# Performance work log

Measured on AMD Instinct MI355X. Metric: run time of the kernel, lower is better.

## Reference

```python
import jax, jax.numpy as jnp
import numpy as np

EPS = 1e-12  # torch F.normalize eps


def setup_inputs() -> dict:
    key = jax.random.key(0)
    k1, k2 = jax.random.split(key)
    b, c, n, h, w = 4, 64, 25, 64, 64
    dims = 64
    x = jax.random.normal(k1, (b, c, n, h, w), dtype=jnp.float32)
    # 1x1 conv weight: Conv2d(channels, dims*3, 1, bias=False) -> [3*dims, channels]
    W = jax.random.normal(k2, (3 * dims, c), dtype=jnp.float32) * 0.05
    return {"x": x, "W": W}


def reference(x, W):
    b, c, n, h, w = x.shape
    N = n * h * w
    # 1x1 conv over channel dim (applied per (b, n) slice == plain channel matmul)
    qkv = jnp.einsum('oc,bcnhw->bonhw', W, x)  # [b, 3d, n, h, w]
    q, k, v = jnp.split(qkv, 3, axis=1)        # each [b, d, n, h, w]
    d = q.shape[1]
    q = q.reshape(b, d, N)  # b c (n h w)
    k = k.reshape(b, d, N)
    v = v.reshape(b, d, N)
    # L2-normalize each channel across the token axis (torch normalize semantics)
    qn = q / jnp.maximum(jnp.linalg.norm(q, axis=-1, keepdims=True), EPS)
    kn = k / jnp.maximum(jnp.linalg.norm(k, axis=-1, keepdims=True), EPS)
    # channel-wise cross-covariance attention: [b, d, d]
    att = jnp.einsum('bdN,beN->bde', qn, kn)
    att = jax.nn.softmax(att, axis=-1)
    out = jnp.einsum('bde,beN->bdN', att, v)   # [b, d, N]
    return out.reshape(b, d, n, h, w)
```

## Files before the change

kernel.cpp:

```cpp
#include <hip/hip_runtime.h>
#include <hip/hip_bf16.h>


#define BATCH 4
#define CH 64
#define NTOK 102400
#define DIM 64

#define NBLK_G 200
#define TOK_PER_G 512
#define GBLK_OUT 320
#define TILES_PER_BLK 5

static const size_t OFF_PART = 0;
static const size_t OFF_G    = (size_t)BATCH * NBLK_G * 4096;
static const size_t OFF_T1   = OFF_G  + (size_t)BATCH * 4096;
static const size_t OFF_INV  = OFF_T1 + (size_t)BATCH * 4096;
static const size_t OFF_MT   = OFF_INV + (size_t)BATCH * 128;
static const size_t WS_FLOATS_FULL = OFF_MT + (size_t)BATCH * 4096;

static const size_t SOFF_G   = 0;
static const size_t SOFF_T1  = (size_t)BATCH * 4096;
static const size_t SOFF_INV = SOFF_T1 + (size_t)BATCH * 4096;
static const size_t SOFF_MT  = SOFF_INV + (size_t)BATCH * 128;

typedef __attribute__((ext_vector_type(8))) short short8v;
typedef __attribute__((ext_vector_type(4))) float f32x4;

__global__ void k_zero(float* __restrict__ p, int n) {
  int i = blockIdx.x * blockDim.x + threadIdx.x;
  if (i < n) p[i] = 0.f;
}

__device__ __forceinline__ short f2bf(float f) {
  unsigned u = __builtin_bit_cast(unsigned, f);
  unsigned r = (u + 0x7fffu + ((u >> 16) & 1u)) >> 16;
  return (short)r;
}
__device__ __forceinline__ float bf2f(short s) {
  unsigned u = ((unsigned)(unsigned short)s) << 16;
  return __builtin_bit_cast(float, u);
}

template <bool ATOMIC>
__global__ __launch_bounds__(256, 3) void k_gram(const float* __restrict__ x,
                                                 float* __restrict__ dstG) {
  __shared__ short his[2][4096];
  __shared__ short los[2][4096];
  __shared__ float p2t[64][65];
  const int b = blockIdx.y, blk = blockIdx.x;
  const int tid = threadIdx.x;
  const int w = tid >> 6, lane = tid & 63;
  const int col = lane & 15, kh = lane >> 4;
  const int cs = tid >> 2, tq = tid & 3;

  const float* xb = x + (size_t)b * CH * NTOK;
  const int t0 = blk * TOK_PER_G;

  f32x4 a1[4], a2[4];
#pragma unroll
  for (int cb = 0; cb < 4; ++cb)
#pragma unroll
    for (int r = 0; r < 4; ++r) { a1[cb][r] = 0.f; a2[cb][r] = 0.f; }

  const int sbase = cs * 64;
  const int s0 = ((2 * tq) ^ (cs & 7)) << 3;
  const int s1 = ((2 * tq + 1) ^ (cs & 7)) << 3;

  {
    const float* src = xb + (size_t)cs * NTOK + t0 + 16 * tq;
    float4 v0 = *(const float4*)(src);
    float4 v1 = *(const float4*)(src + 4);
    float4 v2 = *(const float4*)(src + 8);
    float4 v3 = *(const float4*)(src + 12);
    float f[16] = {v0.x, v0.y, v0.z, v0.w, v1.x, v1.y, v1.z, v1.w,
                   v2.x, v2.y, v2.z, v2.w, v3.x, v3.y, v3.z, v3.w};
    short8v h01, h23, l01, l23;
#pragma unroll
    for (int j = 0; j < 8; ++j) {
      short h = f2bf(f[j]);     h01[j] = h; l01[j] = f2bf(f[j] - bf2f(h));
      short g = f2bf(f[j + 8]); h23[j] = g; l23[j] = f2bf(f[j + 8] - bf2f(g));
    }
    *(short8v*)&his[0][sbase + s0] = h01;
    *(short8v*)&his[0][sbase + s1] = h23;
    *(short8v*)&los[0][sbase + s0] = l01;
    *(short8v*)&los[0][sbase + s1] = l23;
  }
  __syncthreads();

#pragma unroll 1
  for (int i = 0; i < TOK_PER_G / 64; ++i) {
    const int cur = i & 1;
    const bool more = (i + 1) < TOK_PER_G / 64;
    float4 n0, n1, n2, n3;
    if (more) {
      const float* src = xb + (size_t)cs * NTOK + t0 + (i + 1) * 64 + 16 * tq;
      n0 = *(const float4*)(src);
      n1 = *(const float4*)(src + 4);
      n2 = *(const float4*)(src + 8);
      n3 = *(const float4*)(src + 12);
    }
    const short* hp = his[cur];
    const short* lp = los[cur];
#pragma unroll
    for (int kc = 0; kc < 2; ++kc) {
      const int g = kc * 4 + kh;
      const int rA = 16 * w + col;
      const short8v A = *(const short8v*)&hp[rA * 64 + ((g ^ (rA & 7)) << 3)];
#pragma unroll
      for (int cb = 0; cb < 4; ++cb) {
        const int rB = 16 * cb + col;
        const int off = rB * 64 + ((g ^ (rB & 7)) << 3);
        const short8v Bh = *(const short8v*)&hp[off];
        const short8v Bl = *(const short8v*)&lp[off];
        a1[cb] = __builtin_amdgcn_mfma_f32_16x16x32_bf16(A, Bh, a1[cb], 0, 0, 0);
        a2[cb] = __builtin_amdgcn_mfma_f32_16x16x32_bf16(A, Bl, a2[cb], 0, 0, 0);
      }
    }
    if (more) {
      const int nxt = cur ^ 1;
      float f[16] = {n0.x, n0.y, n0.z, n0.w, n1.x, n1.y, n1.z, n1.w,
                     n2.x, n2.y, n2.z, n2.w, n3.x, n3.y, n3.z, n3.w};
      short8v h01, h23, l01, l23;
#pragma unroll
      for (int j = 0; j < 8; ++j) {
        short h = f2bf(f[j]);     h01[j] = h; l01[j] = f2bf(f[j] - bf2f(h));
        short g2 = f2bf(f[j + 8]); h23[j] = g2; l23[j] = f2bf(f[j + 8] - bf2f(g2));
      }
      *(short8v*)&his[nxt][sbase + s0] = h01;
      *(short8v*)&his[nxt][sbase + s1] = h23;
      *(short8v*)&los[nxt][sbase + s0] = l01;
      *(short8v*)&los[nxt][sbase + s1] = l23;
    }
    __syncthreads();
  }

#pragma unroll
  for (int cb = 0; cb < 4; ++cb)
#pragma unroll
    for (int r = 0; r < 4; ++r)
      p2t[16 * w + 4 * kh + r][16 * cb + col] = a2[cb][r];
  __syncthreads();

  float* dst = ATOMIC ? dstG + (size_t)b * 4096
                      : dstG + ((size_t)(b * NBLK_G + blk)) * 4096;
#pragma unroll
  for (int cb = 0; cb < 4; ++cb) {
#pragma unroll
    for (int r = 0; r < 4; ++r) {
      const int R = 16 * w + 4 * kh + r;
      const int C = 16 * cb + col;
      const float vsum = a1[cb][r] + a2[cb][r] + p2t[C][R];
      if (ATOMIC) atomicAdd(&dst[R * 64 + C], vsum);
      else        dst[R * 64 + C] = vsum;
    }
  }
}

__global__ void k_reduceG(const float* __restrict__ partG, float* __restrict__ G) {
  const int el = blockIdx.x * 256 + threadIdx.x;
  const int b = el >> 12;
  const int e = el & 4095;
  const float* p = partG + (size_t)b * NBLK_G * 4096 + e;
  float s = 0.f;
#pragma unroll 8
  for (int q = 0; q < NBLK_G; ++q) s += p[(size_t)q * 4096];
  G[el] = s;
}

__global__ void k_rows(const float* __restrict__ W, const float* __restrict__ G,
                       float* __restrict__ T1, float* __restrict__ inv) {
  const int r = blockIdx.x;
  const int b = blockIdx.y;
  const int lane = threadIdx.x;
  const float* Wr = W + r * 64;
  const float* Gb = G + (size_t)b * 4096;
  float acc = 0.f;
#pragma unroll 8
  for (int c = 0; c < 64; ++c) acc = fmaf(Wr[c], Gb[c * 64 + lane], acc);
  float p = acc * Wr[lane];
#pragma unroll
  for (int m = 1; m < 64; m <<= 1) p += __shfl_xor(p, m, 64);
  const float nrm = sqrtf(fmaxf(p, 0.f));
  const float iv = 1.f / fmaxf(nrm, 1e-12f);
  if (r < 64) T1[((size_t)b * 64 + r) * 64 + lane] = acc * iv;
  if (lane == 0) inv[b * 128 + r] = iv;
}

__global__ void k_att(const float* __restrict__ W, const float* __restrict__ T1,
                      const float* __restrict__ inv, float* __restrict__ MT) {
  __shared__ float WkT[64][65];
  __shared__ float T1s[16][64];
  __shared__ float att[16][64];
  const int b = blockIdx.y;
  const int d0 = blockIdx.x * 16;
  const int tid = threadIdx.x;
  const int w = tid >> 6;
  const int lane = tid & 63;

#pragma unroll
  for (int r = 0; r < 16; ++r) {
    const int e = w + 4 * r;
    WkT[lane][e] = W[(64 + e) * 64 + lane];
  }
#pragma unroll
  for (int r = 0; r < 4; ++r) {
    const int dd = w + 4 * r;
    T1s[dd][lane] = T1[((size_t)b * 64 + d0 + dd) * 64 + lane];
  }
  __syncthreads();

  const float invk = inv[b * 128 + 64 + lane];
  float a[4];
#pragma unroll
  for (int it = 0; it < 4; ++it) {
    const int dd = 4 * w + it;
    float s = 0.f;
#pragma unroll 8
    for (int c = 0; c < 64; ++c) s = fmaf(T1s[dd][c], WkT[c][lane], s);
    a[it] = s * invk;
  }
#pragma unroll
  for (int it = 0; it < 4; ++it) {
    float m = a[it];
#pragma unroll
    for (int k = 1; k < 64; k <<= 1) m = fmaxf(m, __shfl_xor(m, k, 64));
    const float e = expf(a[it] - m);
    float s = e;
#pragma unroll
    for (int k = 1; k < 64; k <<= 1) s += __shfl_xor(s, k, 64);
    att[4 * w + it][lane] = e / s;
  }
  __syncthreads();
#pragma unroll
  for (int it = 0; it < 4; ++it) {
    const int dd = 4 * w + it;
    float m = 0.f;
#pragma unroll 8
    for (int e = 0; e < 64; ++e) m = fmaf(att[dd][e], W[(128 + e) * 64 + lane], m);
    MT[(size_t)b * 4096 + lane * 64 + (d0 + dd)] = m;
  }
}

__device__ __forceinline__ void stage_lin(const float* __restrict__ xrow0,
                                          float* tile, int w, int lane) {
#pragma unroll
  for (int k = 0; k < 4; ++k) {
    const int chunk = w * 4 + k;
    const int r = chunk * 4 + (lane >> 4);
    const float* g = xrow0 + (size_t)r * NTOK + 4 * (lane & 15);
    float* l = tile + chunk * 256;
    __builtin_amdgcn_global_load_lds((const __attribute__((address_space(1))) void*)g,
                                     (__attribute__((address_space(3))) void*)l,
                                     16, 0, 0);
  }
}

#define VM_WAIT0() do { \
    asm volatile("s_waitcnt vmcnt(0)" ::: "memory"); \
    __builtin_amdgcn_sched_barrier(0); \
    __builtin_amdgcn_s_barrier(); \
  } while (0)

__global__ __launch_bounds__(256, 4) void k_out(const float* __restrict__ x,
                                                const float* __restrict__ MT,
                                                float* __restrict__ out) {
  __shared__ float tiles[2][4096];
  const int b = blockIdx.y, blk = blockIdx.x;
  const int tid = threadIdx.x, w = tid >> 6, lane = tid & 63;
  const int dg = lane & 15, tg = lane >> 4;

  const float* xb = x + (size_t)b * CH * NTOK;
  const float* MTb = MT + (size_t)b * 4096;
  float* ob = out + (size_t)b * DIM * NTOK;
  const int t0 = blk * (TILES_PER_BLK * 64);
  const int tof = 16 * w + 4 * tg;

  stage_lin(xb + t0, tiles[0], w, lane);
  VM_WAIT0();

#pragma unroll 1
  for (int i = 0; i < TILES_PER_BLK; ++i) {
    if (i + 1 < TILES_PER_BLK)
      stage_lin(xb + t0 + 64 * (i + 1), tiles[(i + 1) & 1], w, lane);
    const float* tb = tiles[i & 1];

    float acc[4][4] = {};
#pragma unroll 8
    for (int c = 0; c < 64; ++c) {
      const float4 Am = *(const float4*)(MTb + c * 64 + 4 * dg);
      const float4 Bx = *(const float4*)&tb[c * 64 + tof];
      const float am[4] = {Am.x, Am.y, Am.z, Am.w};
      const float bx[4] = {Bx.x, Bx.y, Bx.z, Bx.w};
#pragma unroll
      for (int u = 0; u < 4; ++u)
#pragma unroll
        for (int v = 0; v < 4; ++v) acc[u][v] = fmaf(am[u], bx[v], acc[u][v]);
    }

    const int tt = t0 + 64 * i + tof;
#pragma unroll
    for (int u = 0; u < 4; ++u) {
      *(float4*)(ob + (size_t)(4 * dg + u) * NTOK + tt) =
          make_float4(acc[u][0], acc[u][1], acc[u][2], acc[u][3]);
    }
    VM_WAIT0();
  }
}

extern "C" void kernel_launch(void* const* d_in, const int* in_sizes, int n_in,
                              void* d_out, int out_size, void* d_ws, size_t ws_size,
                              hipStream_t stream) {
  const float* x = (const float*)d_in[0];
  const float* W = (const float*)d_in[1];
  float* out = (float*)d_out;
  float* ws = (float*)d_ws;

  if (ws_size >= WS_FLOATS_FULL * sizeof(float)) {
    float* partG = ws + OFF_PART;
    float* G = ws + OFF_G;
    float* T1 = ws + OFF_T1;
    float* inv = ws + OFF_INV;
    float* MT = ws + OFF_MT;
    k_gram<false><<<dim3(NBLK_G, BATCH), 256, 0, stream>>>(x, partG);
    k_reduceG<<<dim3(64), 256, 0, stream>>>(partG, G);
    k_rows<<<dim3(128, BATCH), 64, 0, stream>>>(W, G, T1, inv);
    k_att<<<dim3(4, BATCH), 256, 0, stream>>>(W, T1, inv, MT);
    k_out<<<dim3(GBLK_OUT, BATCH), 256, 0, stream>>>(x, MT, out);
  } else {
    float* G = ws + SOFF_G;
    float* T1 = ws + SOFF_T1;
    float* inv = ws + SOFF_INV;
    float* MT = ws + SOFF_MT;
    k_zero<<<dim3(64), 256, 0, stream>>>(G, BATCH * 4096);
    k_gram<true><<<dim3(NBLK_G, BATCH), 256, 0, stream>>>(x, G);
    k_rows<<<dim3(128, BATCH), 64, 0, stream>>>(W, G, T1, inv);
    k_att<<<dim3(4, BATCH), 256, 0, stream>>>(W, T1, inv, MT);
    k_out<<<dim3(GBLK_OUT, BATCH), 256, 0, stream>>>(x, MT, out);
  }
}
```

Baseline: 284.8 us.

## Rewrite output GEMM as per-lane token columns with wave-uniform scalar MT loads

The output projection kernel drops the LDS double-buffered tiling. Each wave now handles 64 tokens, one per lane, accumulating all 64 output channels in registers. The MT matrix is read through wave-uniform addresses, so it can come from scalar loads, and x is read directly with coalesced global loads. The Gram reduction launch also changes to 256 blocks of 64 threads for more parallelism. The new kernel needs many registers and has no explicit latency hiding for the x loads, relying on occupancy instead.

```diff
diff --git a/kernel.cpp b/kernel.cpp
--- a/kernel.cpp
+++ b/kernel.cpp
@@ -9,8 +9,6 @@
 
 #define NBLK_G 200
 #define TOK_PER_G 512
-#define GBLK_OUT 320
-#define TILES_PER_BLK 5
 
 static const size_t OFF_PART = 0;
 static const size_t OFF_G    = (size_t)BATCH * NBLK_G * 4096;
@@ -158,7 +156,7 @@
 }
 
 __global__ void k_reduceG(const float* __restrict__ partG, float* __restrict__ G) {
-  const int el = blockIdx.x * 256 + threadIdx.x;
+  const int el = blockIdx.x * 64 + threadIdx.x;
   const int b = el >> 12;
   const int e = el & 4095;
   const float* p = partG + (size_t)b * NBLK_G * 4096 + e;
@@ -242,69 +240,35 @@
   }
 }
 
-__device__ __forceinline__ void stage_lin(const float* __restrict__ xrow0,
-                                          float* tile, int w, int lane) {
-#pragma unroll
-  for (int k = 0; k < 4; ++k) {
-    const int chunk = w * 4 + k;
-    const int r = chunk * 4 + (lane >> 4);
-    const float* g = xrow0 + (size_t)r * NTOK + 4 * (lane & 15);
-    float* l = tile + chunk * 256;
-    __builtin_amdgcn_global_load_lds((const __attribute__((address_space(1))) void*)g,
-                                     (__attribute__((address_space(3))) void*)l,
-                                     16, 0, 0);
-  }
-}
-
-#define VM_WAIT0() do { \
-    asm volatile("s_waitcnt vmcnt(0)" ::: "memory"); \
-    __builtin_amdgcn_sched_barrier(0); \
-    __builtin_amdgcn_s_barrier(); \
-  } while (0)
-
-__global__ __launch_bounds__(256, 4) void k_out(const float* __restrict__ x,
-                                                const float* __restrict__ MT,
-                                                float* __restrict__ out) {
-  __shared__ float tiles[2][4096];
-  const int b = blockIdx.y, blk = blockIdx.x;
-  const int tid = threadIdx.x, w = tid >> 6, lane = tid & 63;
-  const int dg = lane & 15, tg = lane >> 4;
-
-  const float* xb = x + (size_t)b * CH * NTOK;
-  const float* MTb = MT + (size_t)b * 4096;
-  float* ob = out + (size_t)b * DIM * NTOK;
-  const int t0 = blk * (TILES_PER_BLK * 64);
-  const int tof = 16 * w + 4 * tg;
-
-  stage_lin(xb + t0, tiles[0], w, lane);
-  VM_WAIT0();
+__global__ __launch_bounds__(256) void k_out(const float* __restrict__ x,
+                                             const float* __restrict__ MT,
+                                             float* __restrict__ out) {
+  const int wgid = blockIdx.x * 4 + (threadIdx.x >> 6);
+  const int lane = threadIdx.x & 63;
 
 #pragma unroll 1
-  for (int i = 0; i < TILES_PER_BLK; ++i) {
-    if (i + 1 < TILES_PER_BLK)
-      stage_lin(xb + t0 + 64 * (i + 1), tiles[(i + 1) & 1], w, lane);
-    const float* tb = tiles[i & 1];
-
-    float acc[4][4] = {};
-#pragma unroll 8
+  for (int rep = 0; rep < 2; ++rep) {
+    const int tb = __builtin_amdgcn_readfirstlane(wgid * 2 + rep);
+    const int b = tb / 1600;
+    const int t0 = (tb - b * 1600) * 64;
+    const float* xb = x + (size_t)b * CH * NTOK + t0 + lane;
+    const float* Mb = MT + (size_t)b * 4096;
+    float* ob = out + (size_t)b * DIM * NTOK + t0 + lane;
+
+    float acc[64];
+#pragma unroll
+    for (int d = 0; d < 64; ++d) acc[d] = 0.f;
+
+#pragma unroll 4
     for (int c = 0; c < 64; ++c) {
-      const float4 Am = *(const float4*)(MTb + c * 64 + 4 * dg);
-      const float4 Bx = *(const float4*)&tb[c * 64 + tof];
-      const float am[4] = {Am.x, Am.y, Am.z, Am.w};
-      const float bx[4] = {Bx.x, Bx.y, Bx.z, Bx.w};
-#pragma unroll
-      for (int u = 0; u < 4; ++u)
-#pragma unroll
-        for (int v = 0; v < 4; ++v) acc[u][v] = fmaf(am[u], bx[v], acc[u][v]);
-    }
-
-    const int tt = t0 + 64 * i + tof;
-#pragma unroll
-    for (int u = 0; u < 4; ++u) {
-      *(float4*)(ob + (size_t)(4 * dg + u) * NTOK + tt) =
-          make_float4(acc[u][0], acc[u][1], acc[u][2], acc[u][3]);
-    }
-    VM_WAIT0();
+      const float xv = xb[(size_t)c * NTOK];
+      const float* Mc = Mb + c * 64;
+#pragma unroll
+      for (int d = 0; d < 64; ++d) acc[d] = fmaf(Mc[d], xv, acc[d]);
+    }
+
+#pragma unroll
+    for (int d = 0; d < 64; ++d) ob[(size_t)d * NTOK] = acc[d];
   }
 }
 
@@ -323,10 +287,10 @@
     float* inv = ws + OFF_INV;
     float* MT = ws + OFF_MT;
     k_gram<false><<<dim3(NBLK_G, BATCH), 256, 0, stream>>>(x, partG);
-    k_reduceG<<<dim3(64), 256, 0, stream>>>(partG, G);
+    k_reduceG<<<dim3(256), 64, 0, stream>>>(partG, G);
     k_rows<<<dim3(128, BATCH), 64, 0, stream>>>(W, G, T1, inv);
     k_att<<<dim3(4, BATCH), 256, 0, stream>>>(W, T1, inv, MT);
-    k_out<<<dim3(GBLK_OUT, BATCH), 256, 0, stream>>>(x, MT, out);
+    k_out<<<dim3(800), 256, 0, stream>>>(x, MT, out);
   } else {
     float* G = ws + SOFF_G;
     float* T1 = ws + SOFF_T1;
@@ -336,6 +300,6 @@
     k_gram<true><<<dim3(NBLK_G, BATCH), 256, 0, stream>>>(x, G);
     k_rows<<<dim3(128, BATCH), 64, 0, stream>>>(W, G, T1, inv);
     k_att<<<dim3(4, BATCH), 256, 0, stream>>>(W, T1, inv, MT);
-    k_out<<<dim3(GBLK_OUT, BATCH), 256, 0, stream>>>(x, MT, out);
-  }
-}
+    k_out<<<dim3(800), 256, 0, stream>>>(x, MT, out);
+  }
+}
```

After: 275.2 us. 3.4% less time.
